# Kernel tuning notes

Measured on AMD Instinct MI355X. Metric: run time of the kernel, lower is better.

## Reference

```python
import jax, jax.numpy as jnp
import numpy as np

TOPK, ALPHA, BETA, EPS = 13, 1.0, 6.0, 1e-9


def _make_boxes(key, shape, img=640.0):
    k1, k2 = jax.random.split(key)
    xy = jax.random.uniform(k1, shape[:-1] + (2,)) * (img - 80.0)
    wh = 10.0 + jax.random.uniform(k2, shape[:-1] + (2,)) * 70.0
    return jnp.concatenate([xy, xy + wh], axis=-1)


def setup_inputs() -> dict:
    key = jax.random.key(0)
    ks = jax.random.split(key, 8)
    B, L, C, n, K = 32, 8400, 1, 50, 17
    pred_scores = jax.random.uniform(ks[0], (B, L, C))
    pred_bboxes = _make_boxes(ks[1], (B, L, 4))
    pred_poses = jax.random.normal(ks[2], (B, L, K, 3))
    anchor_points = jax.random.uniform(ks[3], (L, 2)) * 640.0
    gt_labels = jax.random.randint(ks[4], (B, n, 1), 0, C)
    gt_bboxes = _make_boxes(ks[5], (B, n, 4))
    gt_poses = jax.random.normal(ks[6], (B, n, K, 3))
    pad_gt_mask = (jax.random.uniform(ks[7], (B, n, 1)) < 0.8).astype(jnp.float32)
    return dict(pred_scores=pred_scores, pred_bboxes=pred_bboxes, pred_poses=pred_poses,
                anchor_points=anchor_points, gt_labels=gt_labels, gt_bboxes=gt_bboxes,
                gt_poses=gt_poses, pad_gt_mask=pad_gt_mask, bg_index=1)


def _batch_iou(b1, b2):
    # b1: [B,n,4], b2: [B,L,4] (x1y1x2y2) -> [B,n,L]
    b1 = b1[:, :, None, :]
    b2 = b2[:, None, :, :]
    xy_min = jnp.maximum(b1[..., :2], b2[..., :2])
    xy_max = jnp.minimum(b1[..., 2:], b2[..., 2:])
    wh = jnp.clip(xy_max - xy_min, 0.0)
    inter = wh[..., 0] * wh[..., 1]
    a1 = (b1[..., 2] - b1[..., 0]) * (b1[..., 3] - b1[..., 1])
    a2 = (b2[..., 2] - b2[..., 0]) * (b2[..., 3] - b2[..., 1])
    union = a1 + a2 - inter
    return inter / (union + EPS)


def _points_in_boxes(points, bboxes):
    # points [L,2], bboxes [B,n,4] -> float [B,n,L]
    xy = points[None, None, :, :]                    # [1,1,L,2]
    lt = xy - bboxes[:, :, None, :2]                 # x - x1, y - y1
    rb = bboxes[:, :, None, 2:] - xy                 # x2 - x, y2 - y
    delta = jnp.concatenate([lt, rb], axis=-1)       # [B,n,L,4]
    return (delta.min(axis=-1) > EPS).astype(bboxes.dtype)


def _gather_topk(metrics, topk, topk_mask):
    # metrics [B,n,L], topk_mask [B,n,1] -> one-hot-per-gt topk mask [B,n,L]
    B, n, L = metrics.shape
    _, idxs = jax.lax.top_k(metrics, topk)           # [B,n,k]
    mask = jnp.broadcast_to(topk_mask > 0, idxs.shape)
    idxs = jnp.where(mask, idxs, 0)
    flat = jnp.zeros((B * n, L), metrics.dtype)
    flat = flat.at[jnp.arange(B * n)[:, None], idxs.reshape(B * n, topk)].add(1.0)
    is_in_topk = flat.reshape(B, n, L)
    # entries hit more than once (collisions from masked idx=0) are dropped, as in torch
    return jnp.where(is_in_topk > 1, 0.0, is_in_topk)


def reference(pred_scores, pred_bboxes, pred_poses, anchor_points, gt_labels,
              gt_bboxes, gt_poses, pad_gt_mask, bg_index):
    B, L, C = pred_scores.shape
    n = gt_bboxes.shape[1]
    K = gt_poses.shape[2]

    ious = _batch_iou(gt_bboxes, pred_bboxes)                                  # [B,n,L]
    # class score of each gt's label at every anchor: [B,n,L]
    bbox_cls_scores = pred_scores.transpose(0, 2, 1)[jnp.arange(B)[:, None], gt_labels[..., 0]]
    align = (bbox_cls_scores ** ALPHA) * (ious ** BETA)
    is_in_gts = _points_in_boxes(anchor_points, gt_bboxes)
    is_in_topk = _gather_topk(align * is_in_gts, TOPK, pad_gt_mask)
    mask_pos = is_in_topk * is_in_gts * pad_gt_mask                            # [B,n,L]
    mps = mask_pos.sum(axis=-2)                                                # [B,L]

    # resolve anchors assigned to multiple gts by max IoU (no-op when none)
    is_max_iou = (ious.argmax(axis=-2)[:, None, :] == jnp.arange(n)[None, :, None]).astype(ious.dtype)
    mask_pos = jnp.where(mps[:, None, :] > 1, is_max_iou, mask_pos)
    mps = mask_pos.sum(axis=-2)

    agi = mask_pos.argmax(axis=-2)                                             # [B,L]
    agi_flat = agi + jnp.arange(B, dtype=agi.dtype)[:, None] * n
    assigned_labels = gt_labels.reshape(-1)[agi_flat]
    assigned_labels = jnp.where(mps > 0, assigned_labels, bg_index)
    assigned_bboxes = gt_bboxes.reshape(-1, 4)[agi_flat]                       # [B,L,4]
    assigned_poses = gt_poses.reshape(-1, K, 3)[agi_flat]                      # [B,L,K,3]

    keep = jnp.array([i for i in range(C + 1) if i != bg_index])
    assigned_scores = jax.nn.one_hot(assigned_labels, C + 1)[..., keep]        # [B,L,C]

    align = align * mask_pos
    max_metrics = align.max(axis=-1, keepdims=True)                            # [B,n,1]
    max_ious = (ious * mask_pos).max(axis=-1, keepdims=True)                   # [B,n,1]
    align = align / (max_metrics + EPS) * max_ious
    assigned_scores = assigned_scores * align.max(axis=-2)[..., None]
    return assigned_labels, assigned_bboxes, assigned_poses, assigned_scores, agi_flat
```

## Files before the change

### kernel.cpp

```cpp
#include <hip/hip_runtime.h>

constexpr int NB = 32;
constexpr int NL = 8400;
constexpr int NC = 1;
constexpr int NG = 50;
constexpr int NKP = 17;
constexpr int TOPK = 13;
constexpr int BLTOT = NB * NL;
constexpr int NROW = NB * NG;
constexpr int CAP = 1024;
constexpr int JBLK = (NL + 255) / 256;
constexpr float FEPS = 1e-9f;

typedef float f32x4 __attribute__((ext_vector_type(4)));

__device__ __forceinline__ float iou_gp(const float4 g, const float4 p, float garea) {
    const float ix1 = fmaxf(g.x, p.x), iy1 = fmaxf(g.y, p.y);
    const float ix2 = fminf(g.z, p.z), iy2 = fminf(g.w, p.w);
    const float iw = fmaxf(ix2 - ix1, 0.f), ih = fmaxf(iy2 - iy1, 0.f);
    const float inter = iw * ih;
    const float parea = (p.z - p.x) * (p.w - p.y);
    return inter / (garea + parea - inter + FEPS);
}

__global__ __launch_bounds__(256) void ingts_kernel(
    const float* __restrict__ anchor_points, const float* __restrict__ gt_bboxes,
    const float* __restrict__ pad_gt_mask,
    unsigned long long* __restrict__ ingts, int* __restrict__ cand_cnt,
    int* __restrict__ cand, unsigned long long* __restrict__ claims)
{
    __shared__ float4 gbox[NG];
    __shared__ int gact[NG];
    const int b = blockIdx.x / JBLK;
    const int jb = (blockIdx.x % JBLK) * 256;
    if (threadIdx.x < NG) {
        gbox[threadIdx.x] = reinterpret_cast<const float4*>(gt_bboxes)[b * NG + threadIdx.x];
        gact[threadIdx.x] = pad_gt_mask[b * NG + threadIdx.x] > 0.f;
    }
    __syncthreads();
    const int j = jb + threadIdx.x;
    if (j >= NL) return;
    claims[b * NL + j] = 0ull;
    const float2 a = reinterpret_cast<const float2*>(anchor_points)[j];
    unsigned long long m = 0;
    for (int i = 0; i < NG; ++i) {
        const float4 g = gbox[i];
        const float din = fminf(fminf(a.x - g.x, a.y - g.y), fminf(g.z - a.x, g.w - a.y));
        if (din > FEPS) {
            m |= (1ull << i);
            if (gact[i]) {
                const int row = b * NG + i;
                const int slot = atomicAdd(&cand_cnt[row], 1);
                if (slot < CAP) cand[row * CAP + slot] = j;
            }
        }
    }
    ingts[b * NL + j] = m;
}

__global__ __launch_bounds__(256) void topk_claim_kernel(
    const float* __restrict__ pred_scores, const float* __restrict__ pred_bboxes,
    const int* __restrict__ gt_labels, const float* __restrict__ gt_bboxes,
    const float* __restrict__ pad_gt_mask,
    const unsigned long long* __restrict__ ingts, const int* __restrict__ cand_cnt,
    const int* __restrict__ cand, unsigned long long* __restrict__ claims)
{
    const int row = blockIdx.x * 4 + (threadIdx.x >> 6);
    const int lane = threadIdx.x & 63;
    if (row >= NROW) return;
    if (pad_gt_mask[row] <= 0.f) return;
    const int b = row / NG, i = row % NG;
    const float4 g = reinterpret_cast<const float4*>(gt_bboxes)[row];
    const float garea = (g.z - g.x) * (g.w - g.y);
    const int lab = gt_labels[row];
    const int cnt = min(cand_cnt[row], CAP);

    float v[16]; int jj[16];
    #pragma unroll
    for (int s = 0; s < 16; ++s) {
        float mv = -1.f; int mj = NL + lane;
        const int c = s * 64 + lane;
        if (c < cnt) {
            const int j = cand[row * CAP + c];
            const float4 p = reinterpret_cast<const float4*>(pred_bboxes)[b * NL + j];
            const float iou = iou_gp(g, p, garea);
            const float sc = pred_scores[(b * NL + j) * NC + lab];
            const float i2 = iou * iou;
            mv = sc * i2 * i2 * i2;
            mj = j;
        }
        v[s] = mv; jj[s] = mj;
    }

    int ct = 0;
    for (int t = 0; t < TOPK; ++t) {
        float bv = -1.f; int bj = 0x7fffffff;
        #pragma unroll
        for (int s = 0; s < 16; ++s)
            if (v[s] > bv || (v[s] == bv && jj[s] < bj)) { bv = v[s]; bj = jj[s]; }
        for (int off = 32; off; off >>= 1) {
            const float v2 = __shfl_xor(bv, off);
            const int   j2 = __shfl_xor(bj, off);
            if (v2 > bv || (v2 == bv && j2 < bj)) { bv = v2; bj = j2; }
        }
        if (bv <= 0.f) break;
        if (lane == 0) atomicOr(&claims[b * NL + bj], 1ull << i);
        ++ct;
        #pragma unroll
        for (int s = 0; s < 16; ++s) if (jj[s] == bj) v[s] = -1.f;
    }

    const int needed = TOPK - ct;
    if (needed > 0) {
        int zcum = 0;
        for (int base = 0; base < NL && zcum < needed; base += 64) {
            const int j = base + lane;
            bool zero = false, ing = false;
            if (j < NL) {
                ing = (ingts[b * NL + j] >> i) & 1ull;
                if (!ing) {
                    zero = true;
                } else {
                    const float4 p = reinterpret_cast<const float4*>(pred_bboxes)[b * NL + j];
                    const float iou = iou_gp(g, p, garea);
                    const float sc = pred_scores[(b * NL + j) * NC + lab];
                    const float i2 = iou * iou;
                    zero = (sc * i2 * i2 * i2 == 0.f);
                }
            }
            const unsigned long long bal = __ballot(zero);
            const int rank = zcum + __popcll(bal & ((1ull << lane) - 1ull));
            if (zero && ing && rank < needed)
                atomicOr(&claims[b * NL + j], 1ull << i);
            zcum += __popcll(bal);
        }
    }
}

__global__ __launch_bounds__(256) void resolve_kernel(
    const float* __restrict__ pred_scores, const float* __restrict__ pred_bboxes,
    const int* __restrict__ gt_labels, const float* __restrict__ gt_bboxes,
    const unsigned long long* __restrict__ claims,
    int* __restrict__ agi_arr, float* __restrict__ align_arr,
    unsigned* __restrict__ rma, unsigned* __restrict__ rmi)
{
    const int idx = blockIdx.x * 256 + threadIdx.x;
    if (idx >= BLTOT) return;
    const int b = idx / NL;
    const unsigned long long M = claims[idx];
    const int mps = __popcll(M);
    int agi = -1;
    float av = 0.f;
    if (mps >= 1) {
        const float4 p = reinterpret_cast<const float4*>(pred_bboxes)[idx];
        if (mps == 1) {
            agi = __builtin_ctzll(M);
        } else {
            float best = -1.f;
            for (int i = 0; i < NG; ++i) {
                const float4 g = reinterpret_cast<const float4*>(gt_bboxes)[b * NG + i];
                const float ga = (g.z - g.x) * (g.w - g.y);
                const float iou = iou_gp(g, p, ga);
                if (iou > best) { best = iou; agi = i; }
            }
        }
        const float4 g = reinterpret_cast<const float4*>(gt_bboxes)[b * NG + agi];
        const float ga = (g.z - g.x) * (g.w - g.y);
        const float iou = iou_gp(g, p, ga);
        const int lab = gt_labels[b * NG + agi];
        const float s = pred_scores[idx * NC + lab];
        const float i2 = iou * iou;
        av = s * i2 * i2 * i2;
        atomicMax(&rma[b * NG + agi], __float_as_uint(av));
        atomicMax(&rmi[b * NG + agi], __float_as_uint(iou));
    }
    agi_arr[idx] = agi;
    align_arr[idx] = av;
}

__global__ __launch_bounds__(256) void final_kernel(
    const int* __restrict__ gt_labels, const float* __restrict__ gt_bboxes,
    const float* __restrict__ gt_poses,
    const int* __restrict__ agi_arr, const float* __restrict__ align_arr,
    const unsigned* __restrict__ rma, const unsigned* __restrict__ rmi,
    const int* __restrict__ bg_ptr, float* __restrict__ out)
{
    const int idx = blockIdx.x * 256 + threadIdx.x;
    const int b = idx / NL;
    const int agi = agi_arr[idx];
    const int ag = (agi < 0) ? 0 : agi;
    const int bg = *bg_ptr;
    const int lab = gt_labels[b * NG + ag];

    float* labels = out;
    float* bboxes = out + (size_t)BLTOT;
    float* poses  = out + (size_t)5 * BLTOT;
    float* scores = out + (size_t)56 * BLTOT;
    float* agif   = out + (size_t)57 * BLTOT;

    labels[idx] = (agi >= 0) ? (float)lab : (float)bg;
    reinterpret_cast<float4*>(bboxes)[idx] =
        reinterpret_cast<const float4*>(gt_bboxes)[b * NG + ag];
    agif[idx] = (float)(ag + b * NG);

    float sc = 0.f;
    if (agi >= 0 && lab != bg) {
        const float mm = __uint_as_float(rma[b * NG + agi]);
        const float mi = __uint_as_float(rmi[b * NG + agi]);
        sc = align_arr[idx] / (mm + FEPS) * mi;
    }
    scores[idx] = sc;

    constexpr int NQ = BLTOT * NKP * 3 / 4;
    for (int q = idx; q < NQ; q += BLTOT) {
        const int e0 = q * 4;
        f32x4 o;
        #pragma unroll
        for (int c = 0; c < 4; ++c) {
            const int e = e0 + c;
            const int p = e / (NKP * 3);
            const int r = e - p * (NKP * 3);
            const int pb = p / NL;
            int a = agi_arr[p]; if (a < 0) a = 0;
            o[c] = gt_poses[(pb * NG + a) * (NKP * 3) + r];
        }
        __builtin_nontemporal_store(o, reinterpret_cast<f32x4*>(poses) + q);
    }
}

extern "C" void kernel_launch(void* const* d_in, const int* in_sizes, int n_in,
                              void* d_out, int out_size, void* d_ws, size_t ws_size,
                              hipStream_t stream)
{
    const float* pred_scores   = (const float*)d_in[0];
    const float* pred_bboxes   = (const float*)d_in[1];
    const float* anchor_points = (const float*)d_in[3];
    const int*   gt_labels     = (const int*)d_in[4];
    const float* gt_bboxes     = (const float*)d_in[5];
    const float* gt_poses      = (const float*)d_in[6];
    const float* pad_gt_mask   = (const float*)d_in[7];
    const int*   bg_ptr        = (const int*)d_in[8];

    char* w = (char*)d_ws;
    size_t off = 0;
    unsigned* rma = (unsigned*)(w + off); off += (size_t)NROW * 4;
    unsigned* rmi = (unsigned*)(w + off); off += (size_t)NROW * 4;
    int* cand_cnt = (int*)(w + off); off += (size_t)NROW * 4;
    const size_t zero_bytes = off;
    unsigned long long* claims = (unsigned long long*)(w + off); off += (size_t)BLTOT * 8;
    int*   agi_arr   = (int*)  (w + off); off += (size_t)BLTOT * 4;
    float* align_arr = (float*)(w + off); off += (size_t)BLTOT * 4;
    unsigned long long* ingts = (unsigned long long*)(w + off); off += (size_t)BLTOT * 8;
    int* cand = (int*)(w + off); off += (size_t)NROW * CAP * 4;

    (void)hipMemsetAsync(d_ws, 0, zero_bytes, stream);

    ingts_kernel<<<NB * JBLK, 256, 0, stream>>>(
        anchor_points, gt_bboxes, pad_gt_mask, ingts, cand_cnt, cand, claims);

    topk_claim_kernel<<<(NROW + 3) / 4, 256, 0, stream>>>(
        pred_scores, pred_bboxes, gt_labels, gt_bboxes, pad_gt_mask,
        ingts, cand_cnt, cand, claims);

    resolve_kernel<<<(BLTOT + 255) / 256, 256, 0, stream>>>(
        pred_scores, pred_bboxes, gt_labels, gt_bboxes, claims,
        agi_arr, align_arr, rma, rmi);

    final_kernel<<<BLTOT / 256, 256, 0, stream>>>(
        gt_labels, gt_bboxes, gt_poses, agi_arr, align_arr, rma, rmi, bg_ptr,
        (float*)d_out);
}
```

Baseline: 179.6 us.

## Fuse four assigner kernels into one persistent kernel with grid barriers

Replaces four separate launches with a single persistent kernel of 512 blocks that uses atomic-counter grid barriers between phases. It drops the ingts bitmask buffer by recomputing point-in-box from the anchor points in the fallback path. It also simplifies pose gathering so one agi lookup is done per 4-element vector. The aim is to remove launch gaps and memory traffic, at the risk of barrier spin cost, a deadlock if the blocks are not all co-resident, and less parallelism in the grid-stride phases.

```diff
diff --git a/kernel.cpp b/kernel.cpp
--- a/kernel.cpp
+++ b/kernel.cpp
@@ -10,6 +10,8 @@
 constexpr int NROW = NB * NG;
 constexpr int CAP = 1024;
 constexpr int JBLK = (NL + 255) / 256;
+constexpr int GRID = 512;
+constexpr int GSTRIDE = GRID * 256;
 constexpr float FEPS = 1e-9f;
 
 typedef float f32x4 __attribute__((ext_vector_type(4)));
@@ -23,206 +25,221 @@
     return inter / (garea + parea - inter + FEPS);
 }
 
-__global__ __launch_bounds__(256) void ingts_kernel(
-    const float* __restrict__ anchor_points, const float* __restrict__ gt_bboxes,
-    const float* __restrict__ pad_gt_mask,
-    unsigned long long* __restrict__ ingts, int* __restrict__ cand_cnt,
-    int* __restrict__ cand, unsigned long long* __restrict__ claims)
+__device__ __forceinline__ void grid_barrier(unsigned* __restrict__ cnt, unsigned target) {
+    __syncthreads();
+    if (threadIdx.x == 0) {
+        __threadfence();
+        atomicAdd(cnt, 1u);
+        while (__hip_atomic_load(cnt, __ATOMIC_ACQUIRE, __HIP_MEMORY_SCOPE_AGENT) < target)
+            __builtin_amdgcn_s_sleep(8);
+        __threadfence();
+    }
+    __syncthreads();
+}
+
+__global__ __launch_bounds__(256, 2) void fused_kernel(
+    const float* __restrict__ pred_scores, const float* __restrict__ pred_bboxes,
+    const float* __restrict__ anchor_points, const int* __restrict__ gt_labels,
+    const float* __restrict__ gt_bboxes, const float* __restrict__ gt_poses,
+    const float* __restrict__ pad_gt_mask, const int* __restrict__ bg_ptr,
+    unsigned* __restrict__ barcnt,
+    unsigned long long* __restrict__ claims, int* __restrict__ cand_cnt,
+    int* __restrict__ cand, int* __restrict__ agi_arr, float* __restrict__ align_arr,
+    unsigned* __restrict__ rma, unsigned* __restrict__ rmi,
+    float* __restrict__ out)
 {
-    __shared__ float4 gbox[NG];
-    __shared__ int gact[NG];
-    const int b = blockIdx.x / JBLK;
-    const int jb = (blockIdx.x % JBLK) * 256;
-    if (threadIdx.x < NG) {
-        gbox[threadIdx.x] = reinterpret_cast<const float4*>(gt_bboxes)[b * NG + threadIdx.x];
-        gact[threadIdx.x] = pad_gt_mask[b * NG + threadIdx.x] > 0.f;
-    }
-    __syncthreads();
-    const int j = jb + threadIdx.x;
-    if (j >= NL) return;
-    claims[b * NL + j] = 0ull;
-    const float2 a = reinterpret_cast<const float2*>(anchor_points)[j];
-    unsigned long long m = 0;
-    for (int i = 0; i < NG; ++i) {
-        const float4 g = gbox[i];
-        const float din = fminf(fminf(a.x - g.x, a.y - g.y), fminf(g.z - a.x, g.w - a.y));
-        if (din > FEPS) {
-            m |= (1ull << i);
-            if (gact[i]) {
-                const int row = b * NG + i;
-                const int slot = atomicAdd(&cand_cnt[row], 1);
-                if (slot < CAP) cand[row * CAP + slot] = j;
-            }
-        }
-    }
-    ingts[b * NL + j] = m;
-}
-
-__global__ __launch_bounds__(256) void topk_claim_kernel(
-    const float* __restrict__ pred_scores, const float* __restrict__ pred_bboxes,
-    const int* __restrict__ gt_labels, const float* __restrict__ gt_bboxes,
-    const float* __restrict__ pad_gt_mask,
-    const unsigned long long* __restrict__ ingts, const int* __restrict__ cand_cnt,
-    const int* __restrict__ cand, unsigned long long* __restrict__ claims)
-{
-    const int row = blockIdx.x * 4 + (threadIdx.x >> 6);
-    const int lane = threadIdx.x & 63;
-    if (row >= NROW) return;
-    if (pad_gt_mask[row] <= 0.f) return;
-    const int b = row / NG, i = row % NG;
-    const float4 g = reinterpret_cast<const float4*>(gt_bboxes)[row];
-    const float garea = (g.z - g.x) * (g.w - g.y);
-    const int lab = gt_labels[row];
-    const int cnt = min(cand_cnt[row], CAP);
-
-    float v[16]; int jj[16];
-    #pragma unroll
-    for (int s = 0; s < 16; ++s) {
-        float mv = -1.f; int mj = NL + lane;
-        const int c = s * 64 + lane;
-        if (c < cnt) {
-            const int j = cand[row * CAP + c];
-            const float4 p = reinterpret_cast<const float4*>(pred_bboxes)[b * NL + j];
-            const float iou = iou_gp(g, p, garea);
-            const float sc = pred_scores[(b * NL + j) * NC + lab];
-            const float i2 = iou * iou;
-            mv = sc * i2 * i2 * i2;
-            mj = j;
-        }
-        v[s] = mv; jj[s] = mj;
-    }
-
-    int ct = 0;
-    for (int t = 0; t < TOPK; ++t) {
-        float bv = -1.f; int bj = 0x7fffffff;
-        #pragma unroll
-        for (int s = 0; s < 16; ++s)
-            if (v[s] > bv || (v[s] == bv && jj[s] < bj)) { bv = v[s]; bj = jj[s]; }
-        for (int off = 32; off; off >>= 1) {
-            const float v2 = __shfl_xor(bv, off);
-            const int   j2 = __shfl_xor(bj, off);
-            if (v2 > bv || (v2 == bv && j2 < bj)) { bv = v2; bj = j2; }
-        }
-        if (bv <= 0.f) break;
-        if (lane == 0) atomicOr(&claims[b * NL + bj], 1ull << i);
-        ++ct;
-        #pragma unroll
-        for (int s = 0; s < 16; ++s) if (jj[s] == bj) v[s] = -1.f;
-    }
-
-    const int needed = TOPK - ct;
-    if (needed > 0) {
-        int zcum = 0;
-        for (int base = 0; base < NL && zcum < needed; base += 64) {
-            const int j = base + lane;
-            bool zero = false, ing = false;
+    const int tid = threadIdx.x;
+    const int bid = blockIdx.x;
+    const int gid = bid * 256 + tid;
+
+    {
+        __shared__ float4 gbox[NG];
+        __shared__ int gact[NG];
+        for (int tile = bid; tile < NB * JBLK; tile += GRID) {
+            const int b = tile / JBLK;
+            const int jb = (tile % JBLK) * 256;
+            __syncthreads();
+            if (tid < NG) {
+                gbox[tid] = reinterpret_cast<const float4*>(gt_bboxes)[b * NG + tid];
+                gact[tid] = pad_gt_mask[b * NG + tid] > 0.f;
+            }
+            __syncthreads();
+            const int j = jb + tid;
             if (j < NL) {
-                ing = (ingts[b * NL + j] >> i) & 1ull;
-                if (!ing) {
-                    zero = true;
-                } else {
+                claims[b * NL + j] = 0ull;
+                const float2 a = reinterpret_cast<const float2*>(anchor_points)[j];
+                for (int i = 0; i < NG; ++i) {
+                    const float4 g = gbox[i];
+                    const float din = fminf(fminf(a.x - g.x, a.y - g.y),
+                                            fminf(g.z - a.x, g.w - a.y));
+                    if (din > FEPS && gact[i]) {
+                        const int row = b * NG + i;
+                        const int slot = atomicAdd(&cand_cnt[row], 1);
+                        if (slot < CAP) cand[row * CAP + slot] = j;
+                    }
+                }
+            }
+        }
+    }
+    grid_barrier(barcnt, GRID);
+
+    {
+        const int row = bid * 4 + (tid >> 6);
+        const int lane = tid & 63;
+        if (row < NROW && pad_gt_mask[row] > 0.f) {
+            const int b = row / NG, i = row % NG;
+            const float4 g = reinterpret_cast<const float4*>(gt_bboxes)[row];
+            const float garea = (g.z - g.x) * (g.w - g.y);
+            const int lab = gt_labels[row];
+            const int cnt = min(cand_cnt[row], CAP);
+
+            float v[16]; int jj[16];
+            #pragma unroll
+            for (int s = 0; s < 16; ++s) {
+                float mv = -1.f; int mj = NL + lane;
+                const int c = s * 64 + lane;
+                if (c < cnt) {
+                    const int j = cand[row * CAP + c];
                     const float4 p = reinterpret_cast<const float4*>(pred_bboxes)[b * NL + j];
                     const float iou = iou_gp(g, p, garea);
                     const float sc = pred_scores[(b * NL + j) * NC + lab];
                     const float i2 = iou * iou;
-                    zero = (sc * i2 * i2 * i2 == 0.f);
-                }
-            }
-            const unsigned long long bal = __ballot(zero);
-            const int rank = zcum + __popcll(bal & ((1ull << lane) - 1ull));
-            if (zero && ing && rank < needed)
-                atomicOr(&claims[b * NL + j], 1ull << i);
-            zcum += __popcll(bal);
-        }
-    }
-}
-
-__global__ __launch_bounds__(256) void resolve_kernel(
-    const float* __restrict__ pred_scores, const float* __restrict__ pred_bboxes,
-    const int* __restrict__ gt_labels, const float* __restrict__ gt_bboxes,
-    const unsigned long long* __restrict__ claims,
-    int* __restrict__ agi_arr, float* __restrict__ align_arr,
-    unsigned* __restrict__ rma, unsigned* __restrict__ rmi)
-{
-    const int idx = blockIdx.x * 256 + threadIdx.x;
-    if (idx >= BLTOT) return;
-    const int b = idx / NL;
-    const unsigned long long M = claims[idx];
-    const int mps = __popcll(M);
-    int agi = -1;
-    float av = 0.f;
-    if (mps >= 1) {
-        const float4 p = reinterpret_cast<const float4*>(pred_bboxes)[idx];
-        if (mps == 1) {
-            agi = __builtin_ctzll(M);
-        } else {
-            float best = -1.f;
-            for (int i = 0; i < NG; ++i) {
-                const float4 g = reinterpret_cast<const float4*>(gt_bboxes)[b * NG + i];
-                const float ga = (g.z - g.x) * (g.w - g.y);
-                const float iou = iou_gp(g, p, ga);
-                if (iou > best) { best = iou; agi = i; }
-            }
-        }
-        const float4 g = reinterpret_cast<const float4*>(gt_bboxes)[b * NG + agi];
-        const float ga = (g.z - g.x) * (g.w - g.y);
-        const float iou = iou_gp(g, p, ga);
-        const int lab = gt_labels[b * NG + agi];
-        const float s = pred_scores[idx * NC + lab];
-        const float i2 = iou * iou;
-        av = s * i2 * i2 * i2;
-        atomicMax(&rma[b * NG + agi], __float_as_uint(av));
-        atomicMax(&rmi[b * NG + agi], __float_as_uint(iou));
-    }
-    agi_arr[idx] = agi;
-    align_arr[idx] = av;
-}
-
-__global__ __launch_bounds__(256) void final_kernel(
-    const int* __restrict__ gt_labels, const float* __restrict__ gt_bboxes,
-    const float* __restrict__ gt_poses,
-    const int* __restrict__ agi_arr, const float* __restrict__ align_arr,
-    const unsigned* __restrict__ rma, const unsigned* __restrict__ rmi,
-    const int* __restrict__ bg_ptr, float* __restrict__ out)
-{
-    const int idx = blockIdx.x * 256 + threadIdx.x;
-    const int b = idx / NL;
-    const int agi = agi_arr[idx];
-    const int ag = (agi < 0) ? 0 : agi;
-    const int bg = *bg_ptr;
-    const int lab = gt_labels[b * NG + ag];
+                    mv = sc * i2 * i2 * i2;
+                    mj = j;
+                }
+                v[s] = mv; jj[s] = mj;
+            }
+
+            int ct = 0;
+            for (int t = 0; t < TOPK; ++t) {
+                float bv = -1.f; int bj = 0x7fffffff;
+                #pragma unroll
+                for (int s = 0; s < 16; ++s)
+                    if (v[s] > bv || (v[s] == bv && jj[s] < bj)) { bv = v[s]; bj = jj[s]; }
+                for (int off = 32; off; off >>= 1) {
+                    const float v2 = __shfl_xor(bv, off);
+                    const int   j2 = __shfl_xor(bj, off);
+                    if (v2 > bv || (v2 == bv && j2 < bj)) { bv = v2; bj = j2; }
+                }
+                if (bv <= 0.f) break;
+                if (lane == 0) atomicOr(&claims[b * NL + bj], 1ull << i);
+                ++ct;
+                #pragma unroll
+                for (int s = 0; s < 16; ++s) if (jj[s] == bj) v[s] = -1.f;
+            }
+
+            const int needed = TOPK - ct;
+            if (needed > 0) {
+                int zcum = 0;
+                for (int base = 0; base < NL && zcum < needed; base += 64) {
+                    const int j = base + lane;
+                    bool zero = false, ing = false;
+                    if (j < NL) {
+                        const float2 a = reinterpret_cast<const float2*>(anchor_points)[j];
+                        const float din = fminf(fminf(a.x - g.x, a.y - g.y),
+                                                fminf(g.z - a.x, g.w - a.y));
+                        ing = din > FEPS;
+                        if (!ing) {
+                            zero = true;
+                        } else {
+                            const float4 p = reinterpret_cast<const float4*>(pred_bboxes)[b * NL + j];
+                            const float iou = iou_gp(g, p, garea);
+                            const float sc = pred_scores[(b * NL + j) * NC + lab];
+                            const float i2 = iou * iou;
+                            zero = (sc * i2 * i2 * i2 == 0.f);
+                        }
+                    }
+                    const unsigned long long bal = __ballot(zero);
+                    const int rank = zcum + __popcll(bal & ((1ull << lane) - 1ull));
+                    if (zero && ing && rank < needed)
+                        atomicOr(&claims[b * NL + j], 1ull << i);
+                    zcum += __popcll(bal);
+                }
+            }
+        }
+    }
+    grid_barrier(barcnt, 2 * GRID);
+
+    for (int idx = gid; idx < BLTOT; idx += GSTRIDE) {
+        const int b = idx / NL;
+        const unsigned long long M = claims[idx];
+        const int mps = __popcll(M);
+        int agi = -1;
+        float av = 0.f;
+        if (mps >= 1) {
+            const float4 p = reinterpret_cast<const float4*>(pred_bboxes)[idx];
+            if (mps == 1) {
+                agi = __builtin_ctzll(M);
+            } else {
+                float best = -1.f;
+                for (int i = 0; i < NG; ++i) {
+                    const float4 g = reinterpret_cast<const float4*>(gt_bboxes)[b * NG + i];
+                    const float ga = (g.z - g.x) * (g.w - g.y);
+                    const float iou = iou_gp(g, p, ga);
+                    if (iou > best) { best = iou; agi = i; }
+                }
+            }
+            const float4 g = reinterpret_cast<const float4*>(gt_bboxes)[b * NG + agi];
+            const float ga = (g.z - g.x) * (g.w - g.y);
+            const float iou = iou_gp(g, p, ga);
+            const int lab = gt_labels[b * NG + agi];
+            const float s = pred_scores[idx * NC + lab];
+            const float i2 = iou * iou;
+            av = s * i2 * i2 * i2;
+            atomicMax(&rma[b * NG + agi], __float_as_uint(av));
+            atomicMax(&rmi[b * NG + agi], __float_as_uint(iou));
+        }
+        agi_arr[idx] = agi;
+        align_arr[idx] = av;
+    }
+    grid_barrier(barcnt, 3 * GRID);
 
     float* labels = out;
     float* bboxes = out + (size_t)BLTOT;
     float* poses  = out + (size_t)5 * BLTOT;
     float* scores = out + (size_t)56 * BLTOT;
     float* agif   = out + (size_t)57 * BLTOT;
-
-    labels[idx] = (agi >= 0) ? (float)lab : (float)bg;
-    reinterpret_cast<float4*>(bboxes)[idx] =
-        reinterpret_cast<const float4*>(gt_bboxes)[b * NG + ag];
-    agif[idx] = (float)(ag + b * NG);
-
-    float sc = 0.f;
-    if (agi >= 0 && lab != bg) {
-        const float mm = __uint_as_float(rma[b * NG + agi]);
-        const float mi = __uint_as_float(rmi[b * NG + agi]);
-        sc = align_arr[idx] / (mm + FEPS) * mi;
-    }
-    scores[idx] = sc;
-
-    constexpr int NQ = BLTOT * NKP * 3 / 4;
-    for (int q = idx; q < NQ; q += BLTOT) {
+    const int bg = *bg_ptr;
+
+    for (int idx = gid; idx < BLTOT; idx += GSTRIDE) {
+        const int b = idx / NL;
+        const int agi = agi_arr[idx];
+        const int ag = (agi < 0) ? 0 : agi;
+        const int lab = gt_labels[b * NG + ag];
+
+        labels[idx] = (agi >= 0) ? (float)lab : (float)bg;
+        reinterpret_cast<float4*>(bboxes)[idx] =
+            reinterpret_cast<const float4*>(gt_bboxes)[b * NG + ag];
+        agif[idx] = (float)(ag + b * NG);
+
+        float sc = 0.f;
+        if (agi >= 0 && lab != bg) {
+            const float mm = __uint_as_float(rma[b * NG + agi]);
+            const float mi = __uint_as_float(rmi[b * NG + agi]);
+            sc = align_arr[idx] / (mm + FEPS) * mi;
+        }
+        scores[idx] = sc;
+    }
+
+    constexpr int NQ = BLTOT * (NKP * 3) / 4;
+    constexpr int RL = NKP * 3;
+    for (int q = gid; q < NQ; q += GSTRIDE) {
         const int e0 = q * 4;
+        const int p = e0 / RL;
+        const int r0 = e0 - p * RL;
+        int a0 = agi_arr[p]; if (a0 < 0) a0 = 0;
+        const float* src = &gt_poses[((p / NL) * NG + a0) * RL];
         f32x4 o;
         #pragma unroll
         for (int c = 0; c < 4; ++c) {
-            const int e = e0 + c;
-            const int p = e / (NKP * 3);
-            const int r = e - p * (NKP * 3);
-            const int pb = p / NL;
-            int a = agi_arr[p]; if (a < 0) a = 0;
-            o[c] = gt_poses[(pb * NG + a) * (NKP * 3) + r];
+            const int r = r0 + c;
+            if (r < RL) {
+                o[c] = src[r];
+            } else {
+                const int p1 = p + 1;
+                int a1 = agi_arr[p1]; if (a1 < 0) a1 = 0;
+                o[c] = gt_poses[((p1 / NL) * NG + a1) * RL + (r - RL)];
+            }
         }
         __builtin_nontemporal_store(o, reinterpret_cast<f32x4*>(poses) + q);
     }
@@ -243,30 +260,20 @@
 
     char* w = (char*)d_ws;
     size_t off = 0;
+    unsigned* barcnt = (unsigned*)(w + off); off += 256;
     unsigned* rma = (unsigned*)(w + off); off += (size_t)NROW * 4;
     unsigned* rmi = (unsigned*)(w + off); off += (size_t)NROW * 4;
     int* cand_cnt = (int*)(w + off); off += (size_t)NROW * 4;
     const size_t zero_bytes = off;
     unsigned long long* claims = (unsigned long long*)(w + off); off += (size_t)BLTOT * 8;
-    int*   agi_arr   = (int*)  (w + off); off += (size_t)BLTOT * 4;
+    int*   agi_arr   = (int*)(w + off); off += (size_t)BLTOT * 4;
     float* align_arr = (float*)(w + off); off += (size_t)BLTOT * 4;
-    unsigned long long* ingts = (unsigned long long*)(w + off); off += (size_t)BLTOT * 8;
     int* cand = (int*)(w + off); off += (size_t)NROW * CAP * 4;
 
     (void)hipMemsetAsync(d_ws, 0, zero_bytes, stream);
 
-    ingts_kernel<<<NB * JBLK, 256, 0, stream>>>(
-        anchor_points, gt_bboxes, pad_gt_mask, ingts, cand_cnt, cand, claims);
-
-    topk_claim_kernel<<<(NROW + 3) / 4, 256, 0, stream>>>(
-        pred_scores, pred_bboxes, gt_labels, gt_bboxes, pad_gt_mask,
-        ingts, cand_cnt, cand, claims);
-
-    resolve_kernel<<<(BLTOT + 255) / 256, 256, 0, stream>>>(
-        pred_scores, pred_bboxes, gt_labels, gt_bboxes, claims,
-        agi_arr, align_arr, rma, rmi);
-
-    final_kernel<<<BLTOT / 256, 256, 0, stream>>>(
-        gt_labels, gt_bboxes, gt_poses, agi_arr, align_arr, rma, rmi, bg_ptr,
-        (float*)d_out);
-}
+    fused_kernel<<<GRID, 256, 0, stream>>>(
+        pred_scores, pred_bboxes, anchor_points, gt_labels, gt_bboxes, gt_poses,
+        pad_gt_mask, bg_ptr, barcnt, claims, cand_cnt, cand, agi_arr, align_arr,
+        rma, rmi, (float*)d_out);
+}
```

Measured after the change: 429.6 us. +139.2%, slower.

## Fuse in-box candidate scan into topk kernel and simplify pose gather indexing

Applied to the files above, without the earlier changes.

Removes the separate ingts kernel and its global candidate list and bitmask. Each wavefront now scans all anchors for its GT with a ballot-based compaction into shared memory, and recomputes the in-box test in the fallback path. This drops a kernel launch, the global atomics and the workspace traffic, at the cost of each GT row scanning all 8400 anchors. The memset now covers the claims array. The pose gather loop computes the source row once per vector instead of dividing per element.

```diff
diff --git a/kernel.cpp b/kernel.cpp
--- a/kernel.cpp
+++ b/kernel.cpp
@@ -9,7 +9,6 @@
 constexpr int BLTOT = NB * NL;
 constexpr int NROW = NB * NG;
 constexpr int CAP = 1024;
-constexpr int JBLK = (NL + 255) / 256;
 constexpr float FEPS = 1e-9f;
 
 typedef float f32x4 __attribute__((ext_vector_type(4)));
@@ -23,57 +22,38 @@
     return inter / (garea + parea - inter + FEPS);
 }
 
-__global__ __launch_bounds__(256) void ingts_kernel(
-    const float* __restrict__ anchor_points, const float* __restrict__ gt_bboxes,
-    const float* __restrict__ pad_gt_mask,
-    unsigned long long* __restrict__ ingts, int* __restrict__ cand_cnt,
-    int* __restrict__ cand, unsigned long long* __restrict__ claims)
-{
-    __shared__ float4 gbox[NG];
-    __shared__ int gact[NG];
-    const int b = blockIdx.x / JBLK;
-    const int jb = (blockIdx.x % JBLK) * 256;
-    if (threadIdx.x < NG) {
-        gbox[threadIdx.x] = reinterpret_cast<const float4*>(gt_bboxes)[b * NG + threadIdx.x];
-        gact[threadIdx.x] = pad_gt_mask[b * NG + threadIdx.x] > 0.f;
-    }
-    __syncthreads();
-    const int j = jb + threadIdx.x;
-    if (j >= NL) return;
-    claims[b * NL + j] = 0ull;
-    const float2 a = reinterpret_cast<const float2*>(anchor_points)[j];
-    unsigned long long m = 0;
-    for (int i = 0; i < NG; ++i) {
-        const float4 g = gbox[i];
-        const float din = fminf(fminf(a.x - g.x, a.y - g.y), fminf(g.z - a.x, g.w - a.y));
-        if (din > FEPS) {
-            m |= (1ull << i);
-            if (gact[i]) {
-                const int row = b * NG + i;
-                const int slot = atomicAdd(&cand_cnt[row], 1);
-                if (slot < CAP) cand[row * CAP + slot] = j;
-            }
-        }
-    }
-    ingts[b * NL + j] = m;
-}
-
 __global__ __launch_bounds__(256) void topk_claim_kernel(
     const float* __restrict__ pred_scores, const float* __restrict__ pred_bboxes,
-    const int* __restrict__ gt_labels, const float* __restrict__ gt_bboxes,
-    const float* __restrict__ pad_gt_mask,
-    const unsigned long long* __restrict__ ingts, const int* __restrict__ cand_cnt,
-    const int* __restrict__ cand, unsigned long long* __restrict__ claims)
-{
-    const int row = blockIdx.x * 4 + (threadIdx.x >> 6);
+    const float* __restrict__ anchor_points, const int* __restrict__ gt_labels,
+    const float* __restrict__ gt_bboxes, const float* __restrict__ pad_gt_mask,
+    unsigned long long* __restrict__ claims)
+{
+    __shared__ int cl[4][CAP];
+    const int w = threadIdx.x >> 6;
     const int lane = threadIdx.x & 63;
-    if (row >= NROW) return;
+    const int row = blockIdx.x * 4 + w;
     if (pad_gt_mask[row] <= 0.f) return;
     const int b = row / NG, i = row % NG;
     const float4 g = reinterpret_cast<const float4*>(gt_bboxes)[row];
     const float garea = (g.z - g.x) * (g.w - g.y);
     const int lab = gt_labels[row];
-    const int cnt = min(cand_cnt[row], CAP);
+
+    int cnt = 0;
+    for (int base = 0; base < NL; base += 64) {
+        const int j = base + lane;
+        bool in = false;
+        if (j < NL) {
+            const float2 a = reinterpret_cast<const float2*>(anchor_points)[j];
+            const float din = fminf(fminf(a.x - g.x, a.y - g.y),
+                                    fminf(g.z - a.x, g.w - a.y));
+            in = din > FEPS;
+        }
+        const unsigned long long bal = __ballot(in);
+        const int rank = cnt + __popcll(bal & ((1ull << lane) - 1ull));
+        if (in && rank < CAP) cl[w][rank] = j;
+        cnt += __popcll(bal);
+    }
+    cnt = min(cnt, CAP);
 
     float v[16]; int jj[16];
     #pragma unroll
@@ -81,7 +61,7 @@
         float mv = -1.f; int mj = NL + lane;
         const int c = s * 64 + lane;
         if (c < cnt) {
-            const int j = cand[row * CAP + c];
+            const int j = cl[w][c];
             const float4 p = reinterpret_cast<const float4*>(pred_bboxes)[b * NL + j];
             const float iou = iou_gp(g, p, garea);
             const float sc = pred_scores[(b * NL + j) * NC + lab];
@@ -117,7 +97,10 @@
             const int j = base + lane;
             bool zero = false, ing = false;
             if (j < NL) {
-                ing = (ingts[b * NL + j] >> i) & 1ull;
+                const float2 a = reinterpret_cast<const float2*>(anchor_points)[j];
+                const float din = fminf(fminf(a.x - g.x, a.y - g.y),
+                                        fminf(g.z - a.x, g.w - a.y));
+                ing = din > FEPS;
                 if (!ing) {
                     zero = true;
                 } else {
@@ -211,18 +194,25 @@
     }
     scores[idx] = sc;
 
-    constexpr int NQ = BLTOT * NKP * 3 / 4;
+    constexpr int NQ = BLTOT * (NKP * 3) / 4;
+    constexpr int RL = NKP * 3;
     for (int q = idx; q < NQ; q += BLTOT) {
         const int e0 = q * 4;
+        const int p = e0 / RL;
+        const int r0 = e0 - p * RL;
+        int a0 = agi_arr[p]; if (a0 < 0) a0 = 0;
+        const float* src = &gt_poses[((p / NL) * NG + a0) * RL];
         f32x4 o;
         #pragma unroll
         for (int c = 0; c < 4; ++c) {
-            const int e = e0 + c;
-            const int p = e / (NKP * 3);
-            const int r = e - p * (NKP * 3);
-            const int pb = p / NL;
-            int a = agi_arr[p]; if (a < 0) a = 0;
-            o[c] = gt_poses[(pb * NG + a) * (NKP * 3) + r];
+            const int r = r0 + c;
+            if (r < RL) {
+                o[c] = src[r];
+            } else {
+                const int p1 = p + 1;
+                int a1 = agi_arr[p1]; if (a1 < 0) a1 = 0;
+                o[c] = gt_poses[((p1 / NL) * NG + a1) * RL + (r - RL)];
+            }
         }
         __builtin_nontemporal_store(o, reinterpret_cast<f32x4*>(poses) + q);
     }
@@ -245,22 +235,16 @@
     size_t off = 0;
     unsigned* rma = (unsigned*)(w + off); off += (size_t)NROW * 4;
     unsigned* rmi = (unsigned*)(w + off); off += (size_t)NROW * 4;
-    int* cand_cnt = (int*)(w + off); off += (size_t)NROW * 4;
+    unsigned long long* claims = (unsigned long long*)(w + off); off += (size_t)BLTOT * 8;
     const size_t zero_bytes = off;
-    unsigned long long* claims = (unsigned long long*)(w + off); off += (size_t)BLTOT * 8;
     int*   agi_arr   = (int*)  (w + off); off += (size_t)BLTOT * 4;
     float* align_arr = (float*)(w + off); off += (size_t)BLTOT * 4;
-    unsigned long long* ingts = (unsigned long long*)(w + off); off += (size_t)BLTOT * 8;
-    int* cand = (int*)(w + off); off += (size_t)NROW * CAP * 4;
 
     (void)hipMemsetAsync(d_ws, 0, zero_bytes, stream);
 
-    ingts_kernel<<<NB * JBLK, 256, 0, stream>>>(
-        anchor_points, gt_bboxes, pad_gt_mask, ingts, cand_cnt, cand, claims);
-
-    topk_claim_kernel<<<(NROW + 3) / 4, 256, 0, stream>>>(
-        pred_scores, pred_bboxes, gt_labels, gt_bboxes, pad_gt_mask,
-        ingts, cand_cnt, cand, claims);
+    topk_claim_kernel<<<NROW / 4, 256, 0, stream>>>(
+        pred_scores, pred_bboxes, anchor_points, gt_labels, gt_bboxes,
+        pad_gt_mask, claims);
 
     resolve_kernel<<<(BLTOT + 255) / 256, 256, 0, stream>>>(
         pred_scores, pred_bboxes, gt_labels, gt_bboxes, claims,
```

Measured after the change: 201.4 us. 1.12x slower.
